# Optimization experiments

Hardware: AMD Instinct MI355X
Metric: run time of the kernel (lower is better)

## Reference

```python
import jax, jax.numpy as jnp
import numpy as np

N = 100000   # nodes
E = 1600000  # edges
H = 128      # hidden_dim
B = 4096     # number of root pairs
HOPS = 3


def setup_inputs() -> dict:
    key = jax.random.key(0)
    ks = jax.random.split(key, 12)
    s = 0.05
    return {
        "node_feat": jax.random.normal(ks[0], (N, H), jnp.float32),
        "send_embd": jax.random.normal(ks[1], (N, H), jnp.float32),
        "edge_index": jax.random.randint(ks[2], (2, E), 0, N, dtype=jnp.int32),
        "root_index": jax.random.randint(ks[3], (2 * B,), 0, N, dtype=jnp.int32),
        "agg_by_source": 1,
        "lin1_W": jax.random.normal(ks[4], (2 * H, H), jnp.float32) * s,
        "lin1_b": jnp.zeros((H,), jnp.float32),
        "gat_W": jax.random.normal(ks[5], (HOPS, H, H), jnp.float32) * s,
        "gat_asrc": jax.random.normal(ks[6], (HOPS, H), jnp.float32) * s,
        "gat_adst": jax.random.normal(ks[7], (HOPS, H), jnp.float32) * s,
        "gat_b": jnp.zeros((HOPS, H), jnp.float32),
        "lstm_Wih": jax.random.normal(ks[8], (HOPS, 2 * H, 4 * H), jnp.float32) * s,
        "lstm_Whh": jax.random.normal(ks[9], (HOPS, H, 4 * H), jnp.float32) * s,
        "lstm_b": jnp.zeros((HOPS, 4 * H), jnp.float32),
        "lin2_W": jax.random.normal(ks[10], (H, H), jnp.float32) * s,
        "lin2_b": jnp.zeros((H,), jnp.float32),
    }


def _gat_breadth(x, src, dst, W, a_src, a_dst, b):
    # GATConv(heads=1) followed by tanh (GeniePath Breadth layer)
    xw = x @ W                                  # [N, H]
    e_score = jax.nn.leaky_relu((xw @ a_src)[src] + (xw @ a_dst)[dst], 0.2)  # [E]
    # softmax over incoming edges of each destination node
    m = jax.ops.segment_max(e_score, dst, num_segments=N)
    ex = jnp.exp(e_score - m[dst])
    z = jax.ops.segment_sum(ex, dst, num_segments=N)
    alpha = ex / z[dst]                          # [E]
    agg = jax.ops.segment_sum(alpha[:, None] * xw[src], dst, num_segments=N)
    return jnp.tanh(agg + b)


def _lstm_step(inp, h, c, Wih, Whh, b):
    gates = inp @ Wih + h @ Whh + b              # [N, 4H]
    i, f, g, o = jnp.split(gates, 4, axis=-1)
    c = jax.nn.sigmoid(f) * c + jax.nn.sigmoid(i) * jnp.tanh(g)
    h = jax.nn.sigmoid(o) * jnp.tanh(c)
    return h, c


def reference(node_feat, send_embd, edge_index, root_index, agg_by_source,
              lin1_W, lin1_b, gat_W, gat_asrc, gat_adst, gat_b,
              lstm_Wih, lstm_Whh, lstm_b, lin2_W, lin2_b):
    src, dst = edge_index[0], edge_index[1]
    # Aggregation stage input: concat node embedding with broadcast embedding
    x = jnp.concatenate([node_feat, send_embd], axis=1) @ lin1_W + lin1_b  # [N, H]
    # GeniePathLazy: all breadth (GAT) layers run on the projected input x
    h_tmps = [
        _gat_breadth(x, src, dst, gat_W[i], gat_asrc[i], gat_adst[i], gat_b[i])
        for i in range(HOPS)
    ]
    # Depth: per-node LSTM over the hop axis, input = cat(h_tmp, x_prev)
    h = jnp.zeros_like(x)
    c = jnp.zeros_like(x)
    xs = x
    for i in range(HOPS):
        inp = jnp.concatenate([h_tmps[i], xs], axis=1)   # [N, 2H]
        h, c = _lstm_step(inp, h, c, lstm_Wih[i], lstm_Whh[i], lstm_b[i])
        xs = h
    out = xs @ lin2_W + lin2_b                            # [N, H]
    roots = root_index.reshape(-1, 2)
    src_nodes = roots[:, 0] if agg_by_source else roots[:, 1]
    return out[src_nodes]                                 # [B, H]
```

## Files before the change

kernel.cpp:

```cpp
#include <hip/hip_runtime.h>

constexpr int N  = 100000;
constexpr int E  = 1600000;
constexpr int H  = 128;
constexpr int NB = 4096;
constexpr int HOPS = 3;
constexpr int EPT = 8;

constexpr int WOFF_L1  = 0;
constexpr int WOFF_GAT = 32768;
constexpr int WOFF_CAT = 81920;
constexpr int WOFF_L2  = 671744;
constexpr int WTOT     = 688128;

constexpr size_t ALIGN = 256;
constexpr size_t alup(size_t x) { return (x + ALIGN - 1) & ~(ALIGN - 1); }

constexpr size_t OFF_X       = 0;
constexpr size_t OFF_SSRC    = alup(OFF_X + (size_t)N * H * 4);
constexpr size_t OFF_SDST    = alup(OFF_SSRC + (size_t)3 * N * 4);
constexpr size_t OFF_WVEC    = alup(OFF_SDST + (size_t)3 * N * 4);
constexpr size_t OFF_SELMAP  = alup(OFF_WVEC + 6 * H * 4);
constexpr size_t OFF_NODELST = alup(OFF_SELMAP + (size_t)N * 4);
constexpr size_t OFF_CNT     = alup(OFF_NODELST + NB * 4);
constexpr size_t OFF_DEG     = alup(OFF_CNT + 256);
constexpr size_t OFF_OFFS    = alup(OFF_DEG + NB * 4);
constexpr size_t OFF_CURSOR  = alup(OFF_OFFS + (NB + 1) * 4);
constexpr size_t OFF_ESORT   = alup(OFF_CURSOR + NB * 4);
constexpr size_t OFF_AGGXH   = alup(OFF_ESORT + (size_t)E * 4);
constexpr size_t OFF_AGGXL   = alup(OFF_AGGXH + (size_t)3 * NB * H * 2);
constexpr size_t OFF_XSH     = alup(OFF_AGGXL + (size_t)3 * NB * H * 2);
constexpr size_t OFF_XSL     = alup(OFF_XSH + (size_t)NB * H * 2);
constexpr size_t OFF_L2OUT   = alup(OFF_XSL + (size_t)NB * H * 2);
constexpr size_t OFF_WHI     = alup(OFF_L2OUT + (size_t)NB * H * 4);
constexpr size_t OFF_WLO     = alup(OFF_WHI + (size_t)WTOT * 2);

constexpr size_t OFF_AGGRAW  = OFF_X;
constexpr size_t OFF_WV2     = OFF_X + (size_t)16 * 1024 * 1024;
constexpr size_t OFF_C2     = OFF_WV2 + 6 * 256 * 4;
constexpr size_t OFF_PLIST  = OFF_X + (size_t)20 * 1024 * 1024;

__device__ __forceinline__ float lrelu(float v) { return v > 0.f ? v : 0.2f * v; }
__device__ __forceinline__ float sigmoidf_(float v) { return 1.f / (1.f + __expf(-v)); }

__device__ __forceinline__ unsigned short f2bf(float f) {
  unsigned u = __float_as_uint(f);
  unsigned r = (u + 0x7FFFu + ((u >> 16) & 1u)) >> 16;
  return (unsigned short)r;
}
__device__ __forceinline__ float bf2f(unsigned short h) {
  return __uint_as_float((unsigned)h << 16);
}
__device__ __forceinline__ void split_rne(float f, unsigned short& hi, unsigned short& lo) {
  unsigned short hh = f2bf(f);
  hi = hh;
  lo = f2bf(f - bf2f(hh));
}
__device__ __forceinline__ void split_trunc(float f, short* hi, short* lo) {
  unsigned u = __float_as_uint(f);
  *hi = (short)(u >> 16);
  float r = f - __uint_as_float(u & 0xFFFF0000u);
  *lo = (short)(__float_as_uint(r) >> 16);
}

typedef short bf16x8 __attribute__((ext_vector_type(8)));
typedef float f32x4  __attribute__((ext_vector_type(4)));

#define MFMA3(ACC, AH, AL, BH, BL)                                               \
  ACC = __builtin_amdgcn_mfma_f32_16x16x32_bf16(AH, BH, ACC, 0, 0, 0);           \
  ACC = __builtin_amdgcn_mfma_f32_16x16x32_bf16(AH, BL, ACC, 0, 0, 0);           \
  ACC = __builtin_amdgcn_mfma_f32_16x16x32_bf16(AL, BH, ACC, 0, 0, 0);

#define GLOAD_LDS16(G, L)                                                        \
  __builtin_amdgcn_global_load_lds(                                              \
      (const __attribute__((address_space(1))) void*)(G),                        \
      (__attribute__((address_space(3))) void*)(L), 16, 0, 0)

__global__ void init_ws(int* __restrict__ sel_map, int* __restrict__ deg,
                        int* __restrict__ cursor, int* __restrict__ cnt,
                        int* __restrict__ need_flag) {
  int i = blockIdx.x * 256 + threadIdx.x;
  int stride = gridDim.x * 256;
  for (int n = i; n < N; n += stride) { sel_map[n] = -1; need_flag[n] = 0; }
  for (int n = i; n < NB; n += stride) { deg[n] = 0; cursor[n] = 0; }
  if (i < 64) cnt[i] = 0;
}

__global__ void prep_kernel(const float* __restrict__ gat_W,
                            const float* __restrict__ a_src,
                            const float* __restrict__ a_dst,
                            float* __restrict__ wvec,
                            const float* __restrict__ lin1_W,
                            const float* __restrict__ Wih,
                            const float* __restrict__ Whh,
                            const float* __restrict__ lin2_W,
                            unsigned short* __restrict__ whi,
                            unsigned short* __restrict__ wlo) {
  if (blockIdx.x < 6) {
    int i = blockIdx.x >> 1, which = blockIdx.x & 1;
    int k = threadIdx.x;
    __shared__ float av[H];
    if (k < H) av[k] = which ? a_dst[i * H + k] : a_src[i * H + k];
    __syncthreads();
    if (k >= H) return;
    const float* Wr = gat_W + (size_t)i * H * H + (size_t)k * H;
    float s = 0.f;
    #pragma unroll 8
    for (int j = 0; j < H; j++) s = fmaf(Wr[j], av[j], s);
    wvec[(i * 2 + which) * H + k] = s;
    return;
  }
  int idx = (blockIdx.x - 6) * 256 + threadIdx.x;
  if (idx >= WTOT) return;
  float v;
  if (idx < WOFF_GAT) {
    int rel = idx;
    int e = rel & 7, lane = (rel >> 3) & 63, tile = rel >> 9;
    int nl = lane & 15, quad = lane >> 4;
    int c = tile & 7, t = tile >> 3;
    int n = c * 16 + nl, k = t * 32 + quad * 8 + e;
    v = lin1_W[k * 128 + n];
  } else if (idx < WOFF_CAT) {
    int rel = idx - WOFF_GAT;
    int hop = rel / 16384; rel %= 16384;
    int e = rel & 7, lane = (rel >> 3) & 63, tile = rel >> 9;
    int nl = lane & 15, quad = lane >> 4;
    int c = tile & 7, t = tile >> 3;
    int n = c * 16 + nl, k = t * 32 + quad * 8 + e;
    v = gat_W[hop * 16384 + k * 128 + n];
  } else if (idx < WOFF_L2) {
    int rel = idx - WOFF_CAT;
    int hop = rel / 196608; rel %= 196608;
    int e = rel & 7, lane = (rel >> 3) & 63, tile = rel >> 9;
    int nl = lane & 15, quad = lane >> 4;
    int c = tile & 31, t = tile >> 5;
    int ftile = c >> 2, g = c & 3;
    int col = g * 128 + ftile * 16 + nl;
    int k = t * 32 + quad * 8 + e;
    v = (k < 256) ? Wih[hop * 131072 + k * 512 + col]
                  : Whh[hop * 65536 + (k - 256) * 512 + col];
  } else {
    int rel = idx - WOFF_L2;
    int e = rel & 7, lane = (rel >> 3) & 63, tile = rel >> 9;
    int nl = lane & 15, quad = lane >> 4;
    int c = tile & 7, t = tile >> 3;
    int n = c * 16 + nl, k = t * 32 + quad * 8 + e;
    v = lin2_W[k * 128 + n];
  }
  unsigned short hh, ll;
  split_rne(v, hh, ll);
  whi[idx] = hh;
  wlo[idx] = ll;
}

__global__ void prep2_kernel(const float* __restrict__ lin1_W,
                             const float* __restrict__ lin1_b,
                             const float* __restrict__ wvec,
                             float* __restrict__ wv2, float* __restrict__ c2) {
  int v = blockIdx.x;
  int j = threadIdx.x;
  __shared__ float wv[H];
  if (j < H) wv[j] = wvec[v * H + j];
  __syncthreads();
  const float* Wr = lin1_W + (size_t)j * H;
  float s = 0.f;
  #pragma unroll 8
  for (int m = 0; m < H; m++) s = fmaf(Wr[m], wv[m], s);
  wv2[v * 256 + j] = s;
  if (j == 0) {
    float cc = 0.f;
    for (int m = 0; m < H; m++) cc = fmaf(lin1_b[m], wv[m], cc);
    c2[v] = cc;
  }
}

__global__ void roots_assign(const int* __restrict__ root, const int* __restrict__ aggp,
                             int* __restrict__ sel_map, int* __restrict__ node_list,
                             int* __restrict__ cnt, int* __restrict__ need_flag) {
  int b = blockIdx.x * 256 + threadIdx.x;
  if (b >= NB) return;
  int node = root[2 * b + (aggp[0] ? 0 : 1)];
  need_flag[node] = 1;
  int old = atomicCAS(&sel_map[node], -1, -2);
  if (old == -1) {
    int c = atomicAdd(cnt, 1);
    sel_map[node] = c;
    node_list[c] = node;
  }
}

__global__ void edge_pass1(const int* __restrict__ ei, const int* __restrict__ sel_map,
                           int* __restrict__ deg, int* __restrict__ plist,
                           int* __restrict__ plist_cnt, int* __restrict__ need_flag) {
  __shared__ int lcnt, lbase;
  const int T = gridDim.x * 256;
  const int tid = threadIdx.x, lane = tid & 63;
  if (tid == 0) lcnt = 0;
  __syncthreads();
  const int base = blockIdx.x * 256 + tid;
  int dn[EPT], sn[EPT], pos[EPT];
  #pragma unroll
  for (int k = 0; k < EPT; k++) {
    int e = base + k * T;
    dn[k] = (e < E) ? ei[E + e] : -1;
  }
  #pragma unroll
  for (int k = 0; k < EPT; k++) {
    if (dn[k] >= 0) dn[k] = sel_map[dn[k]];
  }
  #pragma unroll
  for (int k = 0; k < EPT; k++) {
    int e = base + k * T;
    sn[k] = (dn[k] >= 0) ? ei[e] : 0;
  }
  #pragma unroll
  for (int k = 0; k < EPT; k++) {
    bool f = dn[k] >= 0;
    if (f) { atomicAdd(&deg[dn[k]], 1); need_flag[sn[k]] = 1; }
    unsigned long long mask = __ballot(f);
    int wc = __popcll(mask);
    int wb = 0;
    if (lane == 0 && wc > 0) wb = atomicAdd(&lcnt, wc);
    wb = __shfl(wb, 0);
    pos[k] = f ? (wb + __popcll(mask & ((1ull << lane) - 1ull))) : -1;
  }
  __syncthreads();
  if (tid == 0) lbase = (lcnt > 0) ? atomicAdd(plist_cnt, lcnt) : 0;
  __syncthreads();
  #pragma unroll
  for (int k = 0; k < EPT; k++) {
    if (pos[k] >= 0) plist[lbase + pos[k]] = (dn[k] << 17) | sn[k];
  }
}

__global__ __launch_bounds__(1024)
void scan_kernel(const int* __restrict__ deg, int* __restrict__ offs) {
  __shared__ int part[1024];
  int t = threadIdx.x;
  int base = t * 4;
  int v0 = deg[base], v1 = deg[base + 1], v2 = deg[base + 2], v3 = deg[base + 3];
  int s = v0 + v1 + v2 + v3;
  part[t] = s;
  __syncthreads();
  for (int off = 1; off < 1024; off <<= 1) {
    int tmp = (t >= off) ? part[t - off] : 0;
    __syncthreads();
    part[t] += tmp;
    __syncthreads();
  }
  int run = part[t] - s;
  offs[base] = run; run += v0;
  offs[base + 1] = run; run += v1;
  offs[base + 2] = run; run += v2;
  offs[base + 3] = run;
  if (t == 1023) offs[NB] = part[1023];
}

__global__ void edge_pass2(const int* __restrict__ plist, const int* __restrict__ plist_cnt,
                           const int* __restrict__ offs, int* __restrict__ cursor,
                           int* __restrict__ es_sorted) {
  int np = plist_cnt[0];
  for (int i = blockIdx.x * 256 + threadIdx.x; i < np; i += gridDim.x * 256) {
    int pk = plist[i];
    int d = pk >> 17, s = pk & 0x1FFFF;
    int p = atomicAdd(&cursor[d], 1);
    es_sorted[offs[d] + p] = s;
  }
}

__global__ void compact_need(const int* __restrict__ need_flag,
                             int* __restrict__ need_list, int* __restrict__ need_cnt) {
  int i = blockIdx.x * 256 + threadIdx.x;
  bool f = (i < N) && (need_flag[i] != 0);
  unsigned long long mask = __ballot(f);
  int lane = threadIdx.x & 63;
  int wcnt = __popcll(mask);
  int base = 0;
  if (lane == 0 && wcnt > 0) base = atomicAdd(need_cnt, wcnt);
  base = __shfl(base, 0);
  if (f) {
    int prefix = __popcll(mask & ((1ull << lane) - 1ull));
    need_list[base + prefix] = i;
  }
}

__global__ __launch_bounds__(256)
void score_pass(const float* __restrict__ a0, const float* __restrict__ a1,
                const float* __restrict__ wv2, const float* __restrict__ c2,
                float* __restrict__ s_src, float* __restrict__ s_dst,
                const int* __restrict__ need_list, const int* __restrict__ need_cnt) {
  const int nneed = need_cnt[0];
  if (blockIdx.x * 16 >= nneed) return;
  __shared__ float Ws[6 * 256];
  __shared__ float C2s[6];
  const int t = threadIdx.x, lane = t & 63, wave = t >> 6;
  const int nl = lane & 15;
  #pragma unroll
  for (int v = 0; v < 6; v++) Ws[v * 256 + t] = wv2[v * 256 + t];
  if (t < 6) C2s[t] = c2[t];
  __syncthreads();

  int r = blockIdx.x * 16 + wave * 4 + (lane >> 4);
  int row = (r < nneed) ? need_list[r] : -1;
  int rc = (row < 0) ? 0 : row;
  const float* src = (nl < 8) ? (a0 + (size_t)rc * H + nl * 16)
                              : (a1 + (size_t)rc * H + (nl - 8) * 16);
  float4 va[4];
  #pragma unroll
  for (int q = 0; q < 4; q++) va[q] = ((const float4*)src)[q];

  float p[6] = {0.f, 0.f, 0.f, 0.f, 0.f, 0.f};
  #pragma unroll
  for (int q = 0; q < 4; q++) {
    float4 v4 = va[q];
    #pragma unroll
    for (int v = 0; v < 6; v++) {
      float4 w4 = *(const float4*)&Ws[v * 256 + nl * 16 + q * 4];
      p[v] = fmaf(v4.x, w4.x, p[v]);
      p[v] = fmaf(v4.y, w4.y, p[v]);
      p[v] = fmaf(v4.z, w4.z, p[v]);
      p[v] = fmaf(v4.w, w4.w, p[v]);
    }
  }
  #pragma unroll
  for (int m = 1; m < 16; m <<= 1)
    #pragma unroll
    for (int v = 0; v < 6; v++) p[v] += __shfl_xor(p[v], m);
  if (nl == 0 && row >= 0) {
    #pragma unroll
    for (int h3 = 0; h3 < 3; h3++) {
      s_src[h3 * N + row] = p[2 * h3 + 0] + C2s[2 * h3 + 0];
      s_dst[h3 * N + row] = p[2 * h3 + 1] + C2s[2 * h3 + 1];
    }
  }
}

__global__ __launch_bounds__(256)
void gat_node_kernel(const int* __restrict__ node_list, const int* __restrict__ cntp,
                     const int* __restrict__ offs, const int* __restrict__ es_sorted,
                     const float* __restrict__ a0, const float* __restrict__ a1,
                     const float* __restrict__ s_src, const float* __restrict__ s_dst,
                     float* __restrict__ agg_raw) {
  int c = blockIdx.x;
  if (c >= cntp[0]) return;
  int t = threadIdx.x;
  int n = node_list[c];
  float sd0 = s_dst[0 * N + n], sd1 = s_dst[1 * N + n], sd2 = s_dst[2 * N + n];
  int e0 = offs[c], e1 = offs[c + 1];
  float m0 = -1e30f, m1 = -1e30f, m2 = -1e30f;
  for (int e = e0 + t; e < e1; e += 256) {
    int s = es_sorted[e];
    m0 = fmaxf(m0, lrelu(s_src[0 * N + s] + sd0));
    m1 = fmaxf(m1, lrelu(s_src[1 * N + s] + sd1));
    m2 = fmaxf(m2, lrelu(s_src[2 * N + s] + sd2));
  }
  __shared__ float red[3][256];
  red[0][t] = m0; red[1][t] = m1; red[2][t] = m2;
  __syncthreads();
  for (int s2 = 128; s2 > 0; s2 >>= 1) {
    if (t < s2) {
      red[0][t] = fmaxf(red[0][t], red[0][t + s2]);
      red[1][t] = fmaxf(red[1][t], red[1][t + s2]);
      red[2][t] = fmaxf(red[2][t], red[2][t + s2]);
    }
    __syncthreads();
  }
  m0 = red[0][0]; m1 = red[1][0]; m2 = red[2][0];
  float u0 = 0.f, u1 = 0.f, u2 = 0.f, z0 = 0.f, z1 = 0.f, z2 = 0.f;
  for (int e = e0; e < e1; e++) {
    int s = es_sorted[e];
    float xs = (t < 128) ? a0[(size_t)s * H + t] : a1[(size_t)s * H + (t - 128)];
    float ex0 = __expf(lrelu(s_src[0 * N + s] + sd0) - m0);
    float ex1 = __expf(lrelu(s_src[1 * N + s] + sd1) - m1);
    float ex2 = __expf(lrelu(s_src[2 * N + s] + sd2) - m2);
    z0 += ex0; z1 += ex1; z2 += ex2;
    u0 = fmaf(ex0, xs, u0); u1 = fmaf(ex1, xs, u1); u2 = fmaf(ex2, xs, u2);
  }
  size_t cb = (size_t)c * 256 + t;
  bool any = e1 > e0;
  agg_raw[0 * ((size_t)NB * 256) + cb] = any ? u0 / z0 : 0.f;
  agg_raw[1 * ((size_t)NB * 256) + cb] = any ? u1 / z1 : 0.f;
  agg_raw[2 * ((size_t)NB * 256) + cb] = any ? u2 / z2 : 0.f;
}

__global__ __launch_bounds__(256)
void gemm_unified(const float* __restrict__ agg_raw,
                  const float* __restrict__ a0, const float* __restrict__ a1,
                  const int* __restrict__ node_list, const int* __restrict__ cntp,
                  const int* __restrict__ offs,
                  const unsigned short* __restrict__ Bth,
                  const unsigned short* __restrict__ Btl,
                  const float* __restrict__ bias,
                  unsigned short* __restrict__ aggxh, unsigned short* __restrict__ aggxl,
                  unsigned short* __restrict__ xsh, unsigned short* __restrict__ xsl) {
  const int t = threadIdx.x, lane = t & 63, wave = t >> 6;
  const int nl = lane & 15, quad = lane >> 4;
  const int rt = blockIdx.x * 64 + wave * 16;
  const int cnt = cntp[0];

  int gr = rt + nl;
  const float *pA, *pB;
  if (gr < 12288) {
    pA = agg_raw + (size_t)gr * 256;
    pB = pA + 128;
  } else {
    int cc = gr - 12288;
    int node = (cc < cnt) ? node_list[cc] : 0;
    pA = a0 + (size_t)node * H;
    pB = a1 + (size_t)node * H;
  }

  f32x4 acc[8];
  #pragma unroll
  for (int c = 0; c < 8; c++) acc[c] = (f32x4){0.f, 0.f, 0.f, 0.f};

  #pragma unroll
  for (int kt = 0; kt < 8; kt++) {
    const float* p = ((kt < 4) ? pA : pB) + (kt & 3) * 32 + quad * 8;
    bf16x8 ahi, alo;
    {
      float4 v0 = *(const float4*)p;
      float4 v1 = *(const float4*)(p + 4);
      float af[8] = {v0.x, v0.y, v0.z, v0.w, v1.x, v1.y, v1.z, v1.w};
      #pragma unroll
      for (int j = 0; j < 8; j++) {
        short h_, l_;
        split_trunc(af[j], &h_, &l_);
        ahi[j] = h_;
        alo[j] = l_;
      }
    }
    #pragma unroll
    for (int c = 0; c < 8; c++) {
      size_t boff = ((size_t)(kt * 8 + c) * 64 + lane) * 8;
      bf16x8 bh = *(const bf16x8*)(Bth + boff);
      bf16x8 bl = *(const bf16x8*)(Btl + boff);
      MFMA3(acc[c], ahi, alo, bh, bl);
    }
  }

  float bv[8];
  #pragma unroll
  for (int c = 0; c < 8; c++) bv[c] = bias[c * 16 + nl];

  #pragma unroll
  for (int r = 0; r < 4; r++) {
    int g2 = rt + quad * 4 + r;
    if (g2 < 12288) {
      int cc = g2 & 4095, h = g2 >> 12;
      bool he = offs[cc + 1] > offs[cc];
      size_t base = (size_t)h * NB * H + (size_t)cc * H;
      #pragma unroll
      for (int c = 0; c < 8; c++) {
        float val = acc[c][r] + (he ? bv[c] : 0.f);
        unsigned short vh, vl;
        split_rne(val, vh, vl);
        aggxh[base + c * 16 + nl] = vh;
        aggxl[base + c * 16 + nl] = vl;
      }
    } else {
      int cc = g2 - 12288;
      size_t base = (size_t)cc * H;
      #pragma unroll
      for (int c = 0; c < 8; c++) {
        float val = acc[c][r] + bv[c];
        unsigned short vh, vl;
        split_rne(val, vh, vl);
        xsh[base + c * 16 + nl] = vh;
        xsl[base + c * 16 + nl] = vl;
      }
    }
  }
}

__global__ __launch_bounds__(512)
void hops3_fused(const unsigned short* __restrict__ aggxh,
                 const unsigned short* __restrict__ aggxl,
                 const unsigned short* __restrict__ xsh,
                 const unsigned short* __restrict__ xsl,
                 const unsigned short* __restrict__ gWh_all,
                 const unsigned short* __restrict__ gWl_all,
                 const float* __restrict__ gbias_all,
                 const unsigned short* __restrict__ CWh_all,
                 const unsigned short* __restrict__ CWl_all,
                 const float* __restrict__ lbias_all,
                 const unsigned short* __restrict__ L2h,
                 const unsigned short* __restrict__ L2l,
                 const float* __restrict__ lin2_b, float* __restrict__ l2out) {
  __shared__ unsigned short Ah[2][2048], Al[2][2048];
  __shared__ unsigned short Xh[2048], Xl[2048];
  __shared__ unsigned short Th[16 * 136], Tl[16 * 136];
  __shared__ unsigned short Hh[16 * 136], Hl[16 * 136];
  const int t = threadIdx.x, lane = t & 63, wave = t >> 6;
  const int nl = lane & 15, quad = lane >> 4;
  const int r0 = blockIdx.x * 16;
  const int f = wave * 16 + nl;

  const int aj = wave & 3;
  const bool hiArr = wave < 4;
  const int ac = aj * 64 + lane;
  const int arow = ac >> 4, aks = ac & 15;
  const int akg = aks ^ (arow & 7);
  const size_t asrc = (size_t)(r0 + arow) * H + akg * 8;

  GLOAD_LDS16((hiArr ? xsh : xsl) + asrc, (hiArr ? Xh : Xl) + aj * 512);
  GLOAD_LDS16((hiArr ? aggxh : aggxl) + asrc,
              (hiArr ? &Ah[0][0] : &Al[0][0]) + aj * 512);
  asm volatile("s_waitcnt vmcnt(0)" ::: "memory");
  __syncthreads();

  float creg[4] = {0.f, 0.f, 0.f, 0.f};
  f32x4 acc2[4];

  #pragma unroll
  for (int hop = 0; hop < 3; hop++) {
    const int buf = hop & 1;
    if (hop < 2) {
      const unsigned short* sp =
          (hiArr ? aggxh : aggxl) + (size_t)(hop + 1) * NB * H + asrc;
      GLOAD_LDS16(sp, (hiArr ? &Ah[buf ^ 1][0] : &Al[buf ^ 1][0]) + aj * 512);
    }

    const unsigned short* gWh = gWh_all + hop * 16384;
    const unsigned short* gWl = gWl_all + hop * 16384;
    f32x4 acc1 = (f32x4){0.f, 0.f, 0.f, 0.f};
    #pragma unroll
    for (int kt = 0; kt < 4; kt++) {
      int sw = ((((kt << 2) + quad) ^ (nl & 7)) << 3);
      bf16x8 ah = *(const bf16x8*)&Ah[buf][nl * 128 + sw];
      bf16x8 al = *(const bf16x8*)&Al[buf][nl * 128 + sw];
      size_t boff = ((size_t)(kt * 8 + wave) * 64 + lane) * 8;
      bf16x8 bh = *(const bf16x8*)(gWh + boff);
      bf16x8 bl = *(const bf16x8*)(gWl + boff);
      MFMA3(acc1, ah, al, bh, bl);
    }
    {
      float bv = gbias_all[hop * H + f];
      #pragma unroll
      for (int r = 0; r < 4; r++) {
        int rl = quad * 4 + r;
        float v = tanhf(acc1[r] + bv);
        unsigned short vh, vl2;
        split_rne(v, vh, vl2);
        Th[rl * 136 + f] = vh;
        Tl[rl * 136 + f] = vl2;
      }
    }
    __syncthreads();

    const unsigned short* CWh = CWh_all + hop * 196608;
    const unsigned short* CWl = CWl_all + hop * 196608;
    #pragma unroll
    for (int g = 0; g < 4; g++) acc2[g] = (f32x4){0.f, 0.f, 0.f, 0.f};
    #pragma unroll
    for (int kt = 0; kt < 4; kt++) {
      int kk = kt * 32 + quad * 8;
      bf16x8 ah = *(const bf16x8*)&Th[nl * 136 + kk];
      bf16x8 al = *(const bf16x8*)&Tl[nl * 136 + kk];
      #pragma unroll
      for (int g = 0; g < 4; g++) {
        size_t boff = ((size_t)(kt * 32 + wave * 4 + g) * 64 + lane) * 8;
        bf16x8 bh = *(const bf16x8*)(CWh + boff);
        bf16x8 bl = *(const bf16x8*)(CWl + boff);
        MFMA3(acc2[g], ah, al, bh, bl);
      }
    }
    #pragma unroll
    for (int kt = 0; kt < 4; kt++) {
      bf16x8 ah, al;
      if (hop == 0) {
        int sw = ((((kt << 2) + quad) ^ (nl & 7)) << 3);
        ah = *(const bf16x8*)&Xh[nl * 128 + sw];
        al = *(const bf16x8*)&Xl[nl * 128 + sw];
      } else {
        int kk = kt * 32 + quad * 8;
        ah = *(const bf16x8*)&Hh[nl * 136 + kk];
        al = *(const bf16x8*)&Hl[nl * 136 + kk];
      }
      #pragma unroll
      for (int g = 0; g < 4; g++) {
        size_t boff = ((size_t)((kt + 4) * 32 + wave * 4 + g) * 64 + lane) * 8;
        bf16x8 bh = *(const bf16x8*)(CWh + boff);
        bf16x8 bl = *(const bf16x8*)(CWl + boff);
        MFMA3(acc2[g], ah, al, bh, bl);
      }
      if (hop > 0) {
        #pragma unroll
        for (int g = 0; g < 4; g++) {
          size_t boff = ((size_t)((kt + 8) * 32 + wave * 4 + g) * 64 + lane) * 8;
          bf16x8 bh = *(const bf16x8*)(CWh + boff);
          bf16x8 bl = *(const bf16x8*)(CWl + boff);
          MFMA3(acc2[g], ah, al, bh, bl);
        }
      }
    }
    __syncthreads();

    {
      const float* lb = lbias_all + hop * 512;
      float b_i = lb[0 * 128 + f], b_f = lb[1 * 128 + f];
      float b_g = lb[2 * 128 + f], b_o = lb[3 * 128 + f];
      #pragma unroll
      for (int r = 0; r < 4; r++) {
        int rl = quad * 4 + r;
        float gi = acc2[0][r] + b_i;
        float gf = acc2[1][r] + b_f;
        float gg = acc2[2][r] + b_g;
        float go = acc2[3][r] + b_o;
        float cn = sigmoidf_(gf) * creg[r] + sigmoidf_(gi) * tanhf(gg);
        float hn = sigmoidf_(go) * tanhf(cn);
        creg[r] = cn;
        unsigned short vh, vl2;
        split_rne(hn, vh, vl2);
        Hh[rl * 136 + f] = vh;
        Hl[rl * 136 + f] = vl2;
      }
    }
    asm volatile("s_waitcnt vmcnt(0)" ::: "memory");
    __syncthreads();
  }

  f32x4 acc3 = (f32x4){0.f, 0.f, 0.f, 0.f};
  #pragma unroll
  for (int kt = 0; kt < 4; kt++) {
    int kk = kt * 32 + quad * 8;
    bf16x8 ah = *(const bf16x8*)&Hh[nl * 136 + kk];
    bf16x8 al = *(const bf16x8*)&Hl[nl * 136 + kk];
    size_t boff = ((size_t)(kt * 8 + wave) * 64 + lane) * 8;
    bf16x8 bh = *(const bf16x8*)(L2h + boff);
    bf16x8 bl = *(const bf16x8*)(L2l + boff);
    MFMA3(acc3, ah, al, bh, bl);
  }
  {
    float bv = lin2_b[f];
    #pragma unroll
    for (int r = 0; r < 4; r++) {
      int row = r0 + quad * 4 + r;
      l2out[(size_t)row * H + f] = acc3[r] + bv;
    }
  }
}

__global__ void scatter_out(const float* __restrict__ l2out, const int* __restrict__ sel_map,
                            const int* __restrict__ root, const int* __restrict__ aggp,
                            float* __restrict__ out) {
  int id = blockIdx.x * 256 + threadIdx.x;
  if (id >= NB * H) return;
  int b = id >> 7, f = id & 127;
  int node = root[2 * b + (aggp[0] ? 0 : 1)];
  int c = sel_map[node];
  out[id] = l2out[(size_t)c * H + f];
}

extern "C" void kernel_launch(void* const* d_in, const int* in_sizes, int n_in,
                              void* d_out, int out_size, void* d_ws, size_t ws_size,
                              hipStream_t stream) {
  const float* node_feat = (const float*)d_in[0];
  const float* send_embd = (const float*)d_in[1];
  const int*   edge_idx  = (const int*)d_in[2];
  const int*   root_idx  = (const int*)d_in[3];
  const int*   aggp      = (const int*)d_in[4];
  const float* lin1_W    = (const float*)d_in[5];
  const float* lin1_b    = (const float*)d_in[6];
  const float* gat_W     = (const float*)d_in[7];
  const float* gat_asrc  = (const float*)d_in[8];
  const float* gat_adst  = (const float*)d_in[9];
  const float* gat_b     = (const float*)d_in[10];
  const float* lstm_Wih  = (const float*)d_in[11];
  const float* lstm_Whh  = (const float*)d_in[12];
  const float* lstm_b    = (const float*)d_in[13];
  const float* lin2_W    = (const float*)d_in[14];
  const float* lin2_b    = (const float*)d_in[15];
  float* out = (float*)d_out;

  char* ws = (char*)d_ws;
  float* agg_raw = (float*)(ws + OFF_AGGRAW);
  float* wv2     = (float*)(ws + OFF_WV2);
  float* c2      = (float*)(ws + OFF_C2);
  int*   plist   = (int*)(ws + OFF_PLIST);
  float* s_src   = (float*)(ws + OFF_SSRC);
  float* s_dst   = (float*)(ws + OFF_SDST);
  float* wvec    = (float*)(ws + OFF_WVEC);
  int*   sel_map = (int*)(ws + OFF_SELMAP);
  int*   nodelst = (int*)(ws + OFF_NODELST);
  int*   cnt     = (int*)(ws + OFF_CNT);
  int*   deg     = (int*)(ws + OFF_DEG);
  int*   offs    = (int*)(ws + OFF_OFFS);
  int*   cursor  = (int*)(ws + OFF_CURSOR);
  int*   esort   = (int*)(ws + OFF_ESORT);
  unsigned short* aggxh = (unsigned short*)(ws + OFF_AGGXH);
  unsigned short* aggxl = (unsigned short*)(ws + OFF_AGGXL);
  unsigned short* xsh   = (unsigned short*)(ws + OFF_XSH);
  unsigned short* xsl   = (unsigned short*)(ws + OFF_XSL);
  float* l2out   = (float*)(ws + OFF_L2OUT);
  unsigned short* whi = (unsigned short*)(ws + OFF_WHI);
  unsigned short* wlo = (unsigned short*)(ws + OFF_WLO);

  int* need_flag = (int*)(ws + OFF_AGGXH);
  int* need_list = need_flag + N;
  int* need_cnt  = cnt + 1;
  int* plist_cnt = cnt + 2;

  init_ws<<<512, 256, 0, stream>>>(sel_map, deg, cursor, cnt, need_flag);
  prep_kernel<<<6 + (WTOT + 255) / 256, 256, 0, stream>>>(
      gat_W, gat_asrc, gat_adst, wvec, lin1_W, lstm_Wih, lstm_Whh, lin2_W, whi, wlo);
  prep2_kernel<<<6, 256, 0, stream>>>(lin1_W, lin1_b, wvec, wv2, c2);
  roots_assign<<<(NB + 255) / 256, 256, 0, stream>>>(root_idx, aggp, sel_map, nodelst, cnt,
                                                     need_flag);

  const int egrid = (E + 256 * EPT - 1) / (256 * EPT);
  edge_pass1<<<egrid, 256, 0, stream>>>(edge_idx, sel_map, deg, plist, plist_cnt,
                                        need_flag);
  compact_need<<<(N + 255) / 256, 256, 0, stream>>>(need_flag, need_list, need_cnt);
  scan_kernel<<<1, 1024, 0, stream>>>(deg, offs);
  edge_pass2<<<256, 256, 0, stream>>>(plist, plist_cnt, offs, cursor, esort);

  score_pass<<<(N + 15) / 16, 256, 0, stream>>>(
      node_feat, send_embd, wv2, c2, s_src, s_dst, need_list, need_cnt);

  gat_node_kernel<<<NB, 256, 0, stream>>>(nodelst, cnt, offs, esort,
                                          node_feat, send_embd, s_src, s_dst, agg_raw);

  gemm_unified<<<256, 256, 0, stream>>>(
      agg_raw, node_feat, send_embd, nodelst, cnt, offs,
      whi + WOFF_L1, wlo + WOFF_L1, lin1_b,
      aggxh, aggxl, xsh, xsl);

  hops3_fused<<<NB / 16, 512, 0, stream>>>(
      aggxh, aggxl, xsh, xsl,
      whi + WOFF_GAT, wlo + WOFF_GAT, gat_b,
      whi + WOFF_CAT, wlo + WOFF_CAT, lstm_b,
      whi + WOFF_L2, wlo + WOFF_L2, lin2_b, l2out);

  scatter_out<<<(NB * H + 255) / 256, 256, 0, stream>>>(l2out, sel_map, root_idx, aggp, out);
}
```

Before: 321.5 us.

## Stream hop weights through per-wave LDS ring with async global-to-LDS loads

Reworks the fused three-hop GAT+LSTM kernel so each wave streams its weight tiles through a private three-slot LDS ring using global_load_lds. Fine-grained vmcnt waits let the next tile load while the current MFMAs run, replacing direct global B-operand loads. The T and H tiles switch to a swizzled unpadded layout, and the second aggx buffer is dropped in favour of reloading after a barrier. This raises LDS use to roughly 128KB per block, which limits occupancy to one block per CU. Correctness rests on hand-counted vmcnt values that are easy to get wrong.

```diff
diff --git a/kernel.cpp b/kernel.cpp
--- a/kernel.cpp
+++ b/kernel.cpp
@@ -75,6 +75,12 @@
   __builtin_amdgcn_global_load_lds(                                              \
       (const __attribute__((address_space(1))) void*)(G),                        \
       (__attribute__((address_space(3))) void*)(L), 16, 0, 0)
+
+#define VMCNT0  asm volatile("s_waitcnt vmcnt(0)" ::: "memory")
+#define VMCNT4  asm volatile("s_waitcnt vmcnt(4)" ::: "memory")
+#define VMCNT8  asm volatile("s_waitcnt vmcnt(8)" ::: "memory")
+#define VMCNT12 asm volatile("s_waitcnt vmcnt(12)" ::: "memory")
+#define LGKM0   asm volatile("s_waitcnt lgkmcnt(0)" ::: "memory")
 
 __global__ void init_ws(int* __restrict__ sel_map, int* __restrict__ deg,
                         int* __restrict__ cursor, int* __restrict__ cnt,
@@ -473,7 +479,7 @@
   }
 }
 
-__global__ __launch_bounds__(512)
+__global__ __launch_bounds__(512, 1)
 void hops3_fused(const unsigned short* __restrict__ aggxh,
                  const unsigned short* __restrict__ aggxl,
                  const unsigned short* __restrict__ xsh,
@@ -487,14 +493,16 @@
                  const unsigned short* __restrict__ L2h,
                  const unsigned short* __restrict__ L2l,
                  const float* __restrict__ lin2_b, float* __restrict__ l2out) {
-  __shared__ unsigned short Ah[2][2048], Al[2][2048];
-  __shared__ unsigned short Xh[2048], Xl[2048];
-  __shared__ unsigned short Th[16 * 136], Tl[16 * 136];
-  __shared__ unsigned short Hh[16 * 136], Hl[16 * 136];
+  __shared__ unsigned short Ah[2048], Al[2048];
+  __shared__ unsigned short A2h[2048], A2l[2048];
+  __shared__ unsigned short Th_[2048], Tl_[2048];
+  __shared__ unsigned short Hh_[2048], Hl_[2048];
+  __shared__ unsigned short Bst[8][3 * 2048];
   const int t = threadIdx.x, lane = t & 63, wave = t >> 6;
   const int nl = lane & 15, quad = lane >> 4;
   const int r0 = blockIdx.x * 16;
   const int f = wave * 16 + nl;
+  unsigned short* BstW = &Bst[wave][0];
 
   const int aj = wave & 3;
   const bool hiArr = wave < 4;
@@ -503,141 +511,263 @@
   const int akg = aks ^ (arow & 7);
   const size_t asrc = (size_t)(r0 + arow) * H + akg * 8;
 
-  GLOAD_LDS16((hiArr ? xsh : xsl) + asrc, (hiArr ? Xh : Xl) + aj * 512);
-  GLOAD_LDS16((hiArr ? aggxh : aggxl) + asrc,
-              (hiArr ? &Ah[0][0] : &Al[0][0]) + aj * 512);
-  asm volatile("s_waitcnt vmcnt(0)" ::: "memory");
-  __syncthreads();
+  const int fc = f >> 3, fe = f & 7;
+
+  GLOAD_LDS16((hiArr ? aggxh : aggxl) + asrc, (hiArr ? Ah : Al) + aj * 512);
+  GLOAD_LDS16((hiArr ? xsh : xsl) + asrc, (hiArr ? A2h : A2l) + aj * 512);
 
   float creg[4] = {0.f, 0.f, 0.f, 0.f};
   f32x4 acc2[4];
 
-  #pragma unroll
   for (int hop = 0; hop < 3; hop++) {
-    const int buf = hop & 1;
-    if (hop < 2) {
-      const unsigned short* sp =
-          (hiArr ? aggxh : aggxl) + (size_t)(hop + 1) * NB * H + asrc;
-      GLOAD_LDS16(sp, (hiArr ? &Ah[buf ^ 1][0] : &Al[buf ^ 1][0]) + aj * 512);
-    }
-
     const unsigned short* gWh = gWh_all + hop * 16384;
     const unsigned short* gWl = gWl_all + hop * 16384;
-    f32x4 acc1 = (f32x4){0.f, 0.f, 0.f, 0.f};
-    #pragma unroll
-    for (int kt = 0; kt < 4; kt++) {
-      int sw = ((((kt << 2) + quad) ^ (nl & 7)) << 3);
-      bf16x8 ah = *(const bf16x8*)&Ah[buf][nl * 128 + sw];
-      bf16x8 al = *(const bf16x8*)&Al[buf][nl * 128 + sw];
-      size_t boff = ((size_t)(kt * 8 + wave) * 64 + lane) * 8;
-      bf16x8 bh = *(const bf16x8*)(gWh + boff);
-      bf16x8 bl = *(const bf16x8*)(gWl + boff);
-      MFMA3(acc1, ah, al, bh, bl);
-    }
-    {
-      float bv = gbias_all[hop * H + f];
-      #pragma unroll
-      for (int r = 0; r < 4; r++) {
-        int rl = quad * 4 + r;
-        float v = tanhf(acc1[r] + bv);
-        unsigned short vh, vl2;
-        split_rne(v, vh, vl2);
-        Th[rl * 136 + f] = vh;
-        Tl[rl * 136 + f] = vl2;
-      }
-    }
-    __syncthreads();
-
     const unsigned short* CWh = CWh_all + hop * 196608;
     const unsigned short* CWl = CWl_all + hop * 196608;
+    const int KT = (hop == 0) ? 8 : 12;
+    const int NU = 2 * KT;
+
+    LGKM0;
+    float gbv = gbias_all[hop * H + f];
+    float b_i = lbias_all[hop * 512 + 0 * 128 + f];
+    float b_f = lbias_all[hop * 512 + 1 * 128 + f];
+    float b_g = lbias_all[hop * 512 + 2 * 128 + f];
+    float b_o = lbias_all[hop * 512 + 3 * 128 + f];
+    VMCNT0;
+
+    {
+      const unsigned short* b0 = gWh + (0 * 8 + wave) * 512 + lane * 8;
+      const unsigned short* c0 = gWl + (0 * 8 + wave) * 512 + lane * 8;
+      GLOAD_LDS16(b0, BstW);
+      GLOAD_LDS16(c0, BstW + 512);
+      GLOAD_LDS16(b0 + 8 * 512, BstW + 1024);
+      GLOAD_LDS16(c0 + 8 * 512, BstW + 1536);
+      const unsigned short* b2 = gWh + (2 * 8 + wave) * 512 + lane * 8;
+      const unsigned short* c2 = gWl + (2 * 8 + wave) * 512 + lane * 8;
+      GLOAD_LDS16(b2, BstW + 2048);
+      GLOAD_LDS16(c2, BstW + 2560);
+      GLOAD_LDS16(b2 + 8 * 512, BstW + 3072);
+      GLOAD_LDS16(c2 + 8 * 512, BstW + 3584);
+      const unsigned short* b4 = CWh + (0 * 32 + wave * 4 + 0) * 512 + lane * 8;
+      const unsigned short* c4 = CWl + (0 * 32 + wave * 4 + 0) * 512 + lane * 8;
+      GLOAD_LDS16(b4, BstW + 4096);
+      GLOAD_LDS16(c4, BstW + 4608);
+      GLOAD_LDS16(b4 + 512, BstW + 5120);
+      GLOAD_LDS16(c4 + 512, BstW + 5632);
+    }
+    VMCNT12;
+    __builtin_amdgcn_sched_barrier(0);
+    __builtin_amdgcn_s_barrier();
+
+    f32x4 acc1 = (f32x4){0.f, 0.f, 0.f, 0.f};
+    VMCNT8;
+    #pragma unroll
+    for (int kt = 0; kt < 2; kt++) {
+      int asw = nl * 128 + ((((kt << 2) + quad) ^ (nl & 7)) << 3);
+      bf16x8 ah = *(const bf16x8*)(Ah + asw);
+      bf16x8 al = *(const bf16x8*)(Al + asw);
+      bf16x8 bh = *(const bf16x8*)(BstW + kt * 1024 + lane * 8);
+      bf16x8 bl = *(const bf16x8*)(BstW + kt * 1024 + 512 + lane * 8);
+      MFMA3(acc1, ah, al, bh, bl);
+    }
+    {
+      const unsigned short* b = CWh + (0 * 32 + wave * 4 + 2) * 512 + lane * 8;
+      const unsigned short* c = CWl + (0 * 32 + wave * 4 + 2) * 512 + lane * 8;
+      GLOAD_LDS16(b, BstW);
+      GLOAD_LDS16(c, BstW + 512);
+      GLOAD_LDS16(b + 512, BstW + 1024);
+      GLOAD_LDS16(c + 512, BstW + 1536);
+    }
+    VMCNT8;
+    #pragma unroll
+    for (int kt = 2; kt < 4; kt++) {
+      int asw = nl * 128 + ((((kt << 2) + quad) ^ (nl & 7)) << 3);
+      bf16x8 ah = *(const bf16x8*)(Ah + asw);
+      bf16x8 al = *(const bf16x8*)(Al + asw);
+      bf16x8 bh = *(const bf16x8*)(BstW + 2048 + (kt - 2) * 1024 + lane * 8);
+      bf16x8 bl = *(const bf16x8*)(BstW + 2048 + (kt - 2) * 1024 + 512 + lane * 8);
+      MFMA3(acc1, ah, al, bh, bl);
+    }
+    {
+      const unsigned short* b = CWh + (1 * 32 + wave * 4 + 0) * 512 + lane * 8;
+      const unsigned short* c = CWl + (1 * 32 + wave * 4 + 0) * 512 + lane * 8;
+      GLOAD_LDS16(b, BstW + 2048);
+      GLOAD_LDS16(c, BstW + 2560);
+      GLOAD_LDS16(b + 512, BstW + 3072);
+      GLOAD_LDS16(c + 512, BstW + 3584);
+    }
+
+    #pragma unroll
+    for (int r = 0; r < 4; r++) {
+      int rl = quad * 4 + r;
+      float v = tanhf(acc1[r] + gbv);
+      unsigned short vh, vl2;
+      split_rne(v, vh, vl2);
+      int addr = rl * 128 + ((fc ^ (rl & 7)) << 3) + fe;
+      Th_[addr] = vh;
+      Tl_[addr] = vl2;
+    }
+    LGKM0;
+    __builtin_amdgcn_s_barrier();
+
+    if (hop < 2) {
+      GLOAD_LDS16((hiArr ? aggxh : aggxl) + (size_t)(hop + 1) * NB * H + asrc,
+                  (hiArr ? Ah : Al) + aj * 512);
+    }
+
     #pragma unroll
     for (int g = 0; g < 4; g++) acc2[g] = (f32x4){0.f, 0.f, 0.f, 0.f};
-    #pragma unroll
-    for (int kt = 0; kt < 4; kt++) {
-      int kk = kt * 32 + quad * 8;
-      bf16x8 ah = *(const bf16x8*)&Th[nl * 136 + kk];
-      bf16x8 al = *(const bf16x8*)&Tl[nl * 136 + kk];
-      #pragma unroll
-      for (int g = 0; g < 4; g++) {
-        size_t boff = ((size_t)(kt * 32 + wave * 4 + g) * 64 + lane) * 8;
-        bf16x8 bh = *(const bf16x8*)(CWh + boff);
-        bf16x8 bl = *(const bf16x8*)(CWl + boff);
-        MFMA3(acc2[g], ah, al, bh, bl);
+
+    for (int kt = 0; kt < KT - 1; kt++) {
+      const unsigned short *pAh, *pAl;
+      int kk;
+      if (kt < 4)      { pAh = Th_; pAl = Tl_; kk = kt; }
+      else if (kt < 8) { pAh = (hop == 0) ? A2h : Hh_;
+                         pAl = (hop == 0) ? A2l : Hl_; kk = kt - 4; }
+      else             { pAh = Hh_; pAl = Hl_; kk = kt - 8; }
+      int asw = nl * 128 + ((((kk << 2) + quad) ^ (nl & 7)) << 3);
+      bf16x8 ah = *(const bf16x8*)(pAh + asw);
+      bf16x8 al = *(const bf16x8*)(pAl + asw);
+
+      int u = 2 * kt;
+      int s0 = (u + 2) % 3;
+      VMCNT8;
+      {
+        unsigned short* sb = BstW + s0 * 2048;
+        bf16x8 b0h = *(const bf16x8*)(sb + lane * 8);
+        bf16x8 b0l = *(const bf16x8*)(sb + 512 + lane * 8);
+        bf16x8 b1h = *(const bf16x8*)(sb + 1024 + lane * 8);
+        bf16x8 b1l = *(const bf16x8*)(sb + 1536 + lane * 8);
+        MFMA3(acc2[0], ah, al, b0h, b0l);
+        MFMA3(acc2[1], ah, al, b1h, b1l);
       }
-    }
-    #pragma unroll
-    for (int kt = 0; kt < 4; kt++) {
-      bf16x8 ah, al;
-      if (hop == 0) {
-        int sw = ((((kt << 2) + quad) ^ (nl & 7)) << 3);
-        ah = *(const bf16x8*)&Xh[nl * 128 + sw];
-        al = *(const bf16x8*)&Xl[nl * 128 + sw];
-      } else {
-        int kk = kt * 32 + quad * 8;
-        ah = *(const bf16x8*)&Hh[nl * 136 + kk];
-        al = *(const bf16x8*)&Hl[nl * 136 + kk];
+      {
+        const unsigned short* b = CWh + ((kt + 1) * 32 + wave * 4 + 2) * 512 + lane * 8;
+        const unsigned short* c = CWl + ((kt + 1) * 32 + wave * 4 + 2) * 512 + lane * 8;
+        unsigned short* d = BstW + s0 * 2048;
+        GLOAD_LDS16(b, d);
+        GLOAD_LDS16(c, d + 512);
+        GLOAD_LDS16(b + 512, d + 1024);
+        GLOAD_LDS16(c + 512, d + 1536);
       }
-      #pragma unroll
-      for (int g = 0; g < 4; g++) {
-        size_t boff = ((size_t)((kt + 4) * 32 + wave * 4 + g) * 64 + lane) * 8;
-        bf16x8 bh = *(const bf16x8*)(CWh + boff);
-        bf16x8 bl = *(const bf16x8*)(CWl + boff);
-        MFMA3(acc2[g], ah, al, bh, bl);
+      int s1 = (u + 3) % 3;
+      VMCNT8;
+      {
+        unsigned short* sb = BstW + s1 * 2048;
+        bf16x8 b0h = *(const bf16x8*)(sb + lane * 8);
+        bf16x8 b0l = *(const bf16x8*)(sb + 512 + lane * 8);
+        bf16x8 b1h = *(const bf16x8*)(sb + 1024 + lane * 8);
+        bf16x8 b1l = *(const bf16x8*)(sb + 1536 + lane * 8);
+        MFMA3(acc2[2], ah, al, b0h, b0l);
+        MFMA3(acc2[3], ah, al, b1h, b1l);
       }
-      if (hop > 0) {
-        #pragma unroll
-        for (int g = 0; g < 4; g++) {
-          size_t boff = ((size_t)((kt + 8) * 32 + wave * 4 + g) * 64 + lane) * 8;
-          bf16x8 bh = *(const bf16x8*)(CWh + boff);
-          bf16x8 bl = *(const bf16x8*)(CWl + boff);
-          MFMA3(acc2[g], ah, al, bh, bl);
-        }
+      if (kt < KT - 2) {
+        const unsigned short* b = CWh + ((kt + 2) * 32 + wave * 4 + 0) * 512 + lane * 8;
+        const unsigned short* c = CWl + ((kt + 2) * 32 + wave * 4 + 0) * 512 + lane * 8;
+        unsigned short* d = BstW + s1 * 2048;
+        GLOAD_LDS16(b, d);
+        GLOAD_LDS16(c, d + 512);
+        GLOAD_LDS16(b + 512, d + 1024);
+        GLOAD_LDS16(c + 512, d + 1536);
       }
     }
-    __syncthreads();
-
     {
-      const float* lb = lbias_all + hop * 512;
-      float b_i = lb[0 * 128 + f], b_f = lb[1 * 128 + f];
-      float b_g = lb[2 * 128 + f], b_o = lb[3 * 128 + f];
-      #pragma unroll
-      for (int r = 0; r < 4; r++) {
-        int rl = quad * 4 + r;
-        float gi = acc2[0][r] + b_i;
-        float gf = acc2[1][r] + b_f;
-        float gg = acc2[2][r] + b_g;
-        float go = acc2[3][r] + b_o;
-        float cn = sigmoidf_(gf) * creg[r] + sigmoidf_(gi) * tanhf(gg);
-        float hn = sigmoidf_(go) * tanhf(cn);
-        creg[r] = cn;
-        unsigned short vh, vl2;
-        split_rne(hn, vh, vl2);
-        Hh[rl * 136 + f] = vh;
-        Hl[rl * 136 + f] = vl2;
+      int kt = KT - 1;
+      const unsigned short *pAh, *pAl;
+      int kk;
+      if (kt < 4)      { pAh = Th_; pAl = Tl_; kk = kt; }
+      else if (kt < 8) { pAh = (hop == 0) ? A2h : Hh_;
+                         pAl = (hop == 0) ? A2l : Hl_; kk = kt - 4; }
+      else             { pAh = Hh_; pAl = Hl_; kk = kt - 8; }
+      int asw = nl * 128 + ((((kk << 2) + quad) ^ (nl & 7)) << 3);
+      bf16x8 ah = *(const bf16x8*)(pAh + asw);
+      bf16x8 al = *(const bf16x8*)(pAl + asw);
+      int u = 2 * kt;
+      int s0 = (u + 2) % 3, s1 = (u + 3) % 3;
+      VMCNT4;
+      {
+        unsigned short* sb = BstW + s0 * 2048;
+        bf16x8 b0h = *(const bf16x8*)(sb + lane * 8);
+        bf16x8 b0l = *(const bf16x8*)(sb + 512 + lane * 8);
+        bf16x8 b1h = *(const bf16x8*)(sb + 1024 + lane * 8);
+        bf16x8 b1l = *(const bf16x8*)(sb + 1536 + lane * 8);
+        MFMA3(acc2[0], ah, al, b0h, b0l);
+        MFMA3(acc2[1], ah, al, b1h, b1l);
       }
-    }
-    asm volatile("s_waitcnt vmcnt(0)" ::: "memory");
-    __syncthreads();
-  }
-
-  f32x4 acc3 = (f32x4){0.f, 0.f, 0.f, 0.f};
-  #pragma unroll
-  for (int kt = 0; kt < 4; kt++) {
-    int kk = kt * 32 + quad * 8;
-    bf16x8 ah = *(const bf16x8*)&Hh[nl * 136 + kk];
-    bf16x8 al = *(const bf16x8*)&Hl[nl * 136 + kk];
-    size_t boff = ((size_t)(kt * 8 + wave) * 64 + lane) * 8;
-    bf16x8 bh = *(const bf16x8*)(L2h + boff);
-    bf16x8 bl = *(const bf16x8*)(L2l + boff);
-    MFMA3(acc3, ah, al, bh, bl);
-  }
-  {
-    float bv = lin2_b[f];
+      VMCNT0;
+      {
+        unsigned short* sb = BstW + s1 * 2048;
+        bf16x8 b0h = *(const bf16x8*)(sb + lane * 8);
+        bf16x8 b0l = *(const bf16x8*)(sb + 512 + lane * 8);
+        bf16x8 b1h = *(const bf16x8*)(sb + 1024 + lane * 8);
+        bf16x8 b1l = *(const bf16x8*)(sb + 1536 + lane * 8);
+        MFMA3(acc2[2], ah, al, b0h, b0l);
+        MFMA3(acc2[3], ah, al, b1h, b1l);
+      }
+    }
+    LGKM0;
+    __builtin_amdgcn_s_barrier();
+
     #pragma unroll
     for (int r = 0; r < 4; r++) {
-      int row = r0 + quad * 4 + r;
-      l2out[(size_t)row * H + f] = acc3[r] + bv;
-    }
+      int rl = quad * 4 + r;
+      float gi = acc2[0][r] + b_i;
+      float gf = acc2[1][r] + b_f;
+      float gg = acc2[2][r] + b_g;
+      float go = acc2[3][r] + b_o;
+      float cn = sigmoidf_(gf) * creg[r] + sigmoidf_(gi) * tanhf(gg);
+      float hn = sigmoidf_(go) * tanhf(cn);
+      creg[r] = cn;
+      unsigned short vh, vl2;
+      split_rne(hn, vh, vl2);
+      int addr = rl * 128 + ((fc ^ (rl & 7)) << 3) + fe;
+      Hh_[addr] = vh;
+      Hl_[addr] = vl2;
+    }
+  }
+  LGKM0;
+  __builtin_amdgcn_s_barrier();
+
+  float l2bv = lin2_b[f];
+  {
+    const unsigned short* b0 = L2h + (0 * 8 + wave) * 512 + lane * 8;
+    const unsigned short* c0 = L2l + (0 * 8 + wave) * 512 + lane * 8;
+    GLOAD_LDS16(b0, BstW);
+    GLOAD_LDS16(c0, BstW + 512);
+    GLOAD_LDS16(b0 + 8 * 512, BstW + 1024);
+    GLOAD_LDS16(c0 + 8 * 512, BstW + 1536);
+    const unsigned short* b2 = L2h + (2 * 8 + wave) * 512 + lane * 8;
+    const unsigned short* c2 = L2l + (2 * 8 + wave) * 512 + lane * 8;
+    GLOAD_LDS16(b2, BstW + 2048);
+    GLOAD_LDS16(c2, BstW + 2560);
+    GLOAD_LDS16(b2 + 8 * 512, BstW + 3072);
+    GLOAD_LDS16(c2 + 8 * 512, BstW + 3584);
+  }
+  f32x4 acc3 = (f32x4){0.f, 0.f, 0.f, 0.f};
+  VMCNT4;
+  #pragma unroll
+  for (int kt = 0; kt < 2; kt++) {
+    int asw = nl * 128 + ((((kt << 2) + quad) ^ (nl & 7)) << 3);
+    bf16x8 ah = *(const bf16x8*)(Hh_ + asw);
+    bf16x8 al = *(const bf16x8*)(Hl_ + asw);
+    bf16x8 bh = *(const bf16x8*)(BstW + kt * 1024 + lane * 8);
+    bf16x8 bl = *(const bf16x8*)(BstW + kt * 1024 + 512 + lane * 8);
+    MFMA3(acc3, ah, al, bh, bl);
+  }
+  VMCNT0;
+  #pragma unroll
+  for (int kt = 2; kt < 4; kt++) {
+    int asw = nl * 128 + ((((kt << 2) + quad) ^ (nl & 7)) << 3);
+    bf16x8 ah = *(const bf16x8*)(Hh_ + asw);
+    bf16x8 al = *(const bf16x8*)(Hl_ + asw);
+    bf16x8 bh = *(const bf16x8*)(BstW + 2048 + (kt - 2) * 1024 + lane * 8);
+    bf16x8 bl = *(const bf16x8*)(BstW + 2048 + (kt - 2) * 1024 + 512 + lane * 8);
+    MFMA3(acc3, ah, al, bh, bl);
+  }
+  #pragma unroll
+  for (int r = 0; r < 4; r++) {
+    int row = r0 + quad * 4 + r;
+    l2out[(size_t)row * H + f] = acc3[r] + l2bv;
   }
 }
 
```

Result: faster. 311.5 us (-3.1%).
